# Kernel tuning notes

Measured on AMD Instinct MI355X. Metric: run time of the kernel, lower is better.

The kernel has to match this reference:

```python
import jax, jax.numpy as jnp
import numpy as np

B, D, K, UD, E, H = 2048, 256, 20, 512, 64, 256
HID = max(UD, 2 * E)  # FiLM hidden dim = 512
LN_EPS = 1e-5


def setup_inputs() -> dict:
    key = jax.random.key(0)
    ks = jax.random.split(key, 32)
    r = lambda i, shape, s=0.05: jax.random.normal(ks[i], shape, dtype=jnp.float32) * s
    inp = {
        'U': jax.random.normal(ks[0], (B, UD), dtype=jnp.float32),
        'X': jax.random.randint(ks[1], (B, D), 0, K, dtype=jnp.int32),
        # embedding table [K, E]
        'emb': r(2, (K, E), 1.0),
        # u0 linear: e0 = U @ u0_w.T + u0_b
        'u0_w': r(3, (E, UD)), 'u0_b': r(4, (E,)),
        # FiLM gamma branch: Linear(UD->HID), LayerNorm(HID), SiLU, Linear(HID->E)
        'gw1': r(5, (HID, UD)), 'gb1': r(6, (HID,)),
        'gln_w': jnp.ones((HID,), jnp.float32), 'gln_b': jnp.zeros((HID,), jnp.float32),
        'gw2': r(7, (E, HID)), 'gb2': r(8, (E,)),
        # FiLM beta branch
        'bw1': r(9, (HID, UD)), 'bb1': r(10, (HID,)),
        'bln_w': jnp.ones((HID,), jnp.float32), 'bln_b': jnp.zeros((HID,), jnp.float32),
        'bw2': r(11, (E, HID)), 'bb2': r(12, (E,)),
        # 2-layer LSTM (PyTorch gate order i,f,g,o)
        'wih0': r(13, (4 * H, E)), 'whh0': r(14, (4 * H, H)),
        'bih0': r(15, (4 * H,)), 'bhh0': r(16, (4 * H,)),
        'wih1': r(17, (4 * H, H)), 'whh1': r(18, (4 * H, H)),
        'bih1': r(19, (4 * H,)), 'bhh1': r(20, (4 * H,)),
        # output head: logits = h @ head_w.T + head_b
        'head_w': r(21, (K, H)), 'head_b': r(22, (K,)),
    }
    return inp


def _film_branch(u, w1, b1, lnw, lnb, w2, b2):
    h = u @ w1.T + b1
    mu = h.mean(-1, keepdims=True)
    var = ((h - mu) ** 2).mean(-1, keepdims=True)
    h = (h - mu) / jnp.sqrt(var + LN_EPS) * lnw + lnb
    return jax.nn.silu(h) @ w2.T + b2


def _lstm_cell(x, h, c, wih, whh, bih, bhh):
    g = x @ wih.T + bih + h @ whh.T + bhh
    i, f, gg, o = jnp.split(g, 4, axis=-1)
    c = jax.nn.sigmoid(f) * c + jax.nn.sigmoid(i) * jnp.tanh(gg)
    h = jax.nn.sigmoid(o) * jnp.tanh(c)
    return h, c


def reference(U, X, emb, u0_w, u0_b, gw1, gb1, gln_w, gln_b, gw2, gb2,
              bw1, bb1, bln_w, bln_b, bw2, bb2,
              wih0, whh0, bih0, bhh0, wih1, whh1, bih1, bhh1, head_w, head_b):
    # FiLM conditioning from context U
    gam = _film_branch(U, gw1, gb1, gln_w, gln_b, gw2, gb2)  # [B,E]
    bet = _film_branch(U, bw1, bb1, bln_w, bln_b, bw2, bb2)  # [B,E]
    e0 = U @ u0_w.T + u0_b                                   # [B,E] prefix embedding

    # Teacher-forced FiLM-modulated embeddings: e' = e*(1+gamma)+beta
    ex = emb[X] * (1.0 + gam[:, None, :]) + bet[:, None, :]  # [B,D,E]
    xs = jnp.concatenate([e0[:, None, :], ex[:, :-1]], axis=1)  # [B,D,E]
    xs = xs.transpose(1, 0, 2)  # [D,B,E]

    h0 = jnp.zeros((U.shape[0], H), xs.dtype)
    carry0 = (h0, h0, h0, h0)  # (h_l0, c_l0, h_l1, c_l1)

    def step(carry, x_t):
        h_0, c_0, h_1, c_1 = carry
        h_0, c_0 = _lstm_cell(x_t, h_0, c_0, wih0, whh0, bih0, bhh0)
        h_1, c_1 = _lstm_cell(h_0, h_1, c_1, wih1, whh1, bih1, bhh1)
        return (h_1 := h_1, c_1, h_1, c_1) if False else ((h_0, c_0, h_1, c_1), h_1)

    _, hs = jax.lax.scan(step, carry0, xs)  # [D,B,H]

    logits = jnp.einsum('dbh,kh->dbk', hs, head_w) + head_b  # [D,B,K]
    logp = jax.nn.log_softmax(logits, axis=-1)
    tok = X.T[:, :, None]  # [D,B,1]
    logq = jnp.take_along_axis(logp, tok, axis=-1).squeeze(-1).sum(0)  # [B]
    return logq
```

## Files before the change

### kernel.cpp

```cpp
#include <hip/hip_runtime.h>

#define B_   2048
#define D_   256
#define K_   20
#define UD_  512
#define E_   64
#define H_   256
#define HID_ 512

typedef __attribute__((ext_vector_type(8))) short bf8;
typedef __attribute__((ext_vector_type(4))) short s4;
typedef __attribute__((ext_vector_type(4))) float f32x4;
typedef __attribute__((ext_vector_type(4))) float f4;

#define MFMA16(a,b,c) __builtin_amdgcn_mfma_f32_16x16x32_bf16(a, b, c, 0, 0, 0)

#define GLD(dst, p)  asm volatile("global_load_dwordx4 %0, %1, off sc1" : "=v"(dst) : "v"(p))
#define GST2(p, v)   asm volatile("global_store_dwordx2 %0, %1, off sc1" :: "v"(p), "v"(v) : "memory")
#define GSTD(p, v)   asm volatile("global_store_dword %0, %1, off sc1" :: "v"(p), "v"(v) : "memory")
#define GLDD(dst, p) asm volatile("global_load_dword %0, %1, off sc1\n\ts_waitcnt vmcnt(0)" : "=v"(dst) : "v"(p) : "memory")

__device__ __forceinline__ unsigned short f2bf(float x) {
  unsigned u = __float_as_uint(x);
  u += 0x7fffu + ((u >> 16) & 1u);
  return (unsigned short)(u >> 16);
}
__device__ __forceinline__ float bfu(unsigned short x) {
  return __uint_as_float(((unsigned)x) << 16);
}
__device__ __forceinline__ float sigf(float x) {
  return __builtin_amdgcn_rcpf(1.0f + __expf(-x));
}
__device__ __forceinline__ float tanhf_(float x) {
  return 1.0f - 2.0f * __builtin_amdgcn_rcpf(__expf(2.0f * x) + 1.0f);
}

__global__ __launch_bounds__(256) void pack_w(const float* __restrict__ W,
    unsigned short* __restrict__ dst, int NT, int KTsrc, int KTtot, int kt0,
    int ldw, int Nsrc)
{
  int idx = blockIdx.x * 256 + threadIdx.x;
  int total = NT * KTsrc * 64;
  if (idx >= total) return;
  int l  = idx & 63;
  int fk = idx >> 6;
  int kt = fk % KTsrc;
  int nt = fk / KTsrc;
  int n = nt * 16 + (l & 15);
  int k = kt * 32 + ((l >> 4) * 8);
  bf8 o;
#pragma unroll
  for (int j = 0; j < 8; ++j)
    o[j] = (n < Nsrc) ? (short)f2bf(W[(size_t)n * ldw + k + j]) : (short)0;
  *(bf8*)(dst + (((size_t)(nt * KTtot + kt0 + kt)) * 64 + l) * 8) = o;
}

__global__ __launch_bounds__(256) void cvt_bf(const float* __restrict__ src,
    unsigned short* __restrict__ dst, int n8)
{
  int i = blockIdx.x * 256 + threadIdx.x;
  if (i >= n8) return;
  const f4* s = (const f4*)(src + (size_t)i * 8);
  f4 v0 = s[0], v1 = s[1];
  bf8 o;
#pragma unroll
  for (int j = 0; j < 4; ++j) { o[j] = (short)f2bf(v0[j]); o[4 + j] = (short)f2bf(v1[j]); }
  *(bf8*)(dst + (size_t)i * 8) = o;
}

template<bool OUTBF>
__global__ __launch_bounds__(256) void gemm_bt(
    const unsigned short* __restrict__ A, int lda, int aoff,
    const unsigned short* __restrict__ Bp, int KT,
    void* __restrict__ Cptr, int ldc, int coff,
    const float* __restrict__ bias)
{
  int tid = threadIdx.x;
  int l = tid & 63, w = tid >> 6;
  int wr = w >> 1, wc = w & 1;
  int r0 = blockIdx.y * 64 + wr * 32;
  int n0 = blockIdx.x * 64 + wc * 32;
  int lr = l & 15, lk = (l >> 4) * 8;
  f32x4 acc[2][2] = {};
  const unsigned short* a0p = A + (size_t)(r0 + lr) * lda + aoff + lk;
  const unsigned short* a1p = A + (size_t)(r0 + 16 + lr) * lda + aoff + lk;
  int ntb = n0 >> 4;
  for (int kt = 0; kt < KT; ++kt) {
    bf8 a0 = *(const bf8*)(a0p + kt * 32);
    bf8 a1 = *(const bf8*)(a1p + kt * 32);
    bf8 b0 = *(const bf8*)(Bp + (((size_t)(ntb + 0) * KT + kt) * 64 + l) * 8);
    bf8 b1 = *(const bf8*)(Bp + (((size_t)(ntb + 1) * KT + kt) * 64 + l) * 8);
    acc[0][0] = MFMA16(a0, b0, acc[0][0]);
    acc[0][1] = MFMA16(a0, b1, acc[0][1]);
    acc[1][0] = MFMA16(a1, b0, acc[1][0]);
    acc[1][1] = MFMA16(a1, b1, acc[1][1]);
  }
#pragma unroll
  for (int mi = 0; mi < 2; ++mi)
#pragma unroll
  for (int nj = 0; nj < 2; ++nj)
#pragma unroll
  for (int r = 0; r < 4; ++r) {
    int row = r0 + mi * 16 + (l >> 4) * 4 + r;
    int n = n0 + nj * 16 + lr;
    float v = acc[mi][nj][r] + bias[n];
    if (OUTBF) ((unsigned short*)Cptr)[(size_t)row * ldc + coff + n] = f2bf(v);
    else       ((float*)Cptr)[(size_t)row * ldc + coff + n] = v;
  }
}

__global__ __launch_bounds__(256) void ln_silu(
    const float* __restrict__ Hgb, unsigned short* __restrict__ Hsi,
    const float* __restrict__ gw, const float* __restrict__ gb,
    const float* __restrict__ bw, const float* __restrict__ bb)
{
  int tid = threadIdx.x;
  int l = tid & 63, w = tid >> 6;
  int gwv = blockIdx.x * 4 + w;
  int row = gwv >> 1, br = gwv & 1;
  const float* base = Hgb + (size_t)row * 1024 + br * 512 + l * 8;
  f4 v0 = *(const f4*)base;
  f4 v1 = *(const f4*)(base + 4);
  float s1 = 0.f, s2 = 0.f;
#pragma unroll
  for (int j = 0; j < 4; ++j) { s1 += v0[j] + v1[j]; s2 += v0[j] * v0[j] + v1[j] * v1[j]; }
  for (int m = 1; m < 64; m <<= 1) { s1 += __shfl_xor(s1, m, 64); s2 += __shfl_xor(s2, m, 64); }
  float mean = s1 * (1.0f / 512.0f);
  float var  = s2 * (1.0f / 512.0f) - mean * mean;
  float rstd = rsqrtf(var + 1e-5f);
  const float* W  = br ? bw : gw;
  const float* Bb = br ? bb : gb;
  bf8 o;
#pragma unroll
  for (int j = 0; j < 8; ++j) {
    float x = (j < 4) ? v0[j] : v1[j - 4];
    float y = (x - mean) * rstd * W[l * 8 + j] + Bb[l * 8 + j];
    o[j] = (short)f2bf(y * sigf(y));
  }
  *(bf8*)(Hsi + (size_t)row * 1024 + br * 512 + l * 8) = o;
}

struct PParams {
  const unsigned short* embB;
  const unsigned short* gbB;
  const unsigned short* E0;
  const unsigned short* W0p;
  const unsigned short* W1p;
  const unsigned short* Whp;
  unsigned short* H0;
  unsigned short* H1;
  unsigned* flags;
  const float* bih0; const float* bhh0;
  const float* bih1; const float* bhh1;
  const float* headb;
  const int* X;
  float* out;
};

__device__ __forceinline__ bf8 mod_frag(const unsigned short* e,
                                        const unsigned short* gb)
{
  bf8 ev = *(const bf8*)e;
  bf8 gv = *(const bf8*)gb;
  bf8 bv = *(const bf8*)(gb + 64);
  bf8 o;
#pragma unroll
  for (int j = 0; j < 8; ++j) {
    float x = bfu((unsigned short)ev[j]) * (1.0f + bfu((unsigned short)gv[j]))
            + bfu((unsigned short)bv[j]);
    o[j] = (short)f2bf(x);
  }
  return o;
}

__device__ __forceinline__ void group_barrier(unsigned* flags, int gid,
                                              int mem, unsigned target)
{
  asm volatile("s_waitcnt vmcnt(0)" ::: "memory");
  __syncthreads();
  if (threadIdx.x == 0) {
    GSTD(&flags[gid * 16 + mem], target);
  }
  int lane = threadIdx.x & 63;
  if (lane < 16 && lane != mem) {
    const unsigned* fp = &flags[gid * 16 + lane];
    unsigned v;
    GLDD(v, fp);
    while (v < target) {
      __builtin_amdgcn_s_sleep(1);
      GLDD(v, fp);
    }
  }
}

__global__ __launch_bounds__(512, 2) void persistent(PParams P)
{
  __shared__ __align__(16) unsigned short ldsw[120 * 512];
  __shared__ __align__(16) unsigned short tps[8][256];
  const int tid = threadIdx.x;
  const int l = tid & 63, w = tid >> 6;
  const int lr = l & 15, lk = (l >> 4) * 8;
  const int bx = blockIdx.x;
  const int gid = bx & 15;
  const int mem = bx >> 4;

  for (int f = w; f < 104; f += 8) {
    const unsigned short* src;
    if (f < 40) {
      int g = f / 10, kt = f - g * 10;
      src = P.W0p + (((size_t)((g * 16 + mem) * 10 + kt)) * 64 + l) * 8;
    } else {
      int f1 = f - 40; int g = f1 >> 4, kt = f1 & 15;
      src = P.W1p + (((size_t)((g * 16 + mem) * 16 + kt)) * 64 + l) * 8;
    }
    *(bf8*)(ldsw + (size_t)f * 512 + l * 8) = *(const bf8*)src;
  }
  for (int f = w; f < 16; f += 8)
    *(bf8*)(ldsw + (size_t)(104 + f) * 512 + l * 8) =
        *(const bf8*)(P.Whp + ((size_t)f * 64 + l) * 8);
  __syncthreads();

  const int r0 = gid * 128 + w * 16;
  const int c  = mem * 16 + lr;
  const size_t HN = (size_t)B_ * H_;
  const int rowA = r0 + lr;
  const int row2 = l & 15, ch2 = (l >> 4) & 3;
  const size_t strow = (size_t)(r0 + row2) * H_ + mem * 16 + ch2 * 4;
  unsigned short* tb = &tps[w][0];

  const float bi0 = P.bih0[c]           + P.bhh0[c];
  const float bf0 = P.bih0[H_ + c]      + P.bhh0[H_ + c];
  const float bg0 = P.bih0[2 * H_ + c]  + P.bhh0[2 * H_ + c];
  const float bo0 = P.bih0[3 * H_ + c]  + P.bhh0[3 * H_ + c];
  const float bi1 = P.bih1[c]           + P.bhh1[c];
  const float bf1 = P.bih1[H_ + c]      + P.bhh1[H_ + c];
  const float bg1 = P.bih1[2 * H_ + c]  + P.bhh1[2 * H_ + c];
  const float bo1 = P.bih1[3 * H_ + c]  + P.bhh1[3 * H_ + c];
  const float hb0 = P.headb[lr];
  const float hb1 = (lr < 4) ? P.headb[16 + lr] : 0.f;

  float c0r[4] = {};
  float c1r[4] = {};
  float lq[4]  = {};

  for (int ph = 0; ph <= 257; ++ph) {
    const unsigned short* h0r = P.H0 + ((size_t)((ph + 1) & 1)) * HN;
    unsigned short*       h0w = P.H0 + ((size_t)(ph & 1)) * HN;
    const unsigned short* h1r = P.H1 + ((size_t)(ph & 1)) * HN;
    unsigned short*       h1w = P.H1 + ((size_t)((ph + 1) & 1)) * HN;

    bf8 xa[2];
    if (ph < D_) {
      if (ph == 0) {
#pragma unroll
        for (int kt = 0; kt < 2; ++kt)
          xa[kt] = *(const bf8*)(P.E0 + (size_t)rowA * E_ + kt * 32 + lk);
      } else {
        int tok = P.X[rowA * D_ + ph - 1];
#pragma unroll
        for (int kt = 0; kt < 2; ++kt) {
          int k0 = kt * 32 + lk;
          xa[kt] = mod_frag(P.embB + tok * E_ + k0, P.gbB + (size_t)rowA * 128 + k0);
        }
      }
    }
    __builtin_amdgcn_sched_barrier(0);

    bf8 ha[8], h1a[8];
    {
      const unsigned short* pa = h0r + (size_t)rowA * H_ + lk;
#pragma unroll
      for (int kt = 0; kt < 8; ++kt) GLD(ha[kt], pa + kt * 32);
      const unsigned short* pb = h1r + (size_t)rowA * H_ + lk;
#pragma unroll
      for (int kt = 0; kt < 8; ++kt) GLD(h1a[kt], pb + kt * 32);
    }

    f32x4 acc0[4] = {};
    if (ph < D_) {
#pragma unroll
      for (int kt = 0; kt < 2; ++kt)
#pragma unroll
      for (int g = 0; g < 4; ++g) {
        bf8 b = *(const bf8*)(ldsw + (size_t)(g * 10 + kt) * 512 + l * 8);
        acc0[g] = MFMA16(xa[kt], b, acc0[g]);
      }
    }
    asm volatile("s_waitcnt vmcnt(8)" ::: "memory");
    __builtin_amdgcn_sched_barrier(0x100);

    bf8 hv0;
    if (ph < D_) {
#pragma unroll
      for (int kt = 2; kt < 10; ++kt)
#pragma unroll
      for (int g = 0; g < 4; ++g) {
        bf8 b = *(const bf8*)(ldsw + (size_t)(g * 10 + kt) * 512 + l * 8);
        acc0[g] = MFMA16(ha[kt - 2], b, acc0[g]);
      }
#pragma unroll
      for (int r = 0; r < 4; ++r) {
        float iv = sigf(acc0[0][r] + bi0);
        float fv = sigf(acc0[1][r] + bf0);
        float gv = tanhf_(acc0[2][r] + bg0);
        float ov = sigf(acc0[3][r] + bo0);
        float cn = fv * c0r[r] + iv * gv;
        c0r[r] = cn;
        tb[((l >> 4) * 4 + r) * 16 + lr] = f2bf(ov * tanhf_(cn));
      }
      asm volatile("s_waitcnt lgkmcnt(0)" ::: "memory");
      __builtin_amdgcn_sched_barrier(0);
      hv0 = *(const bf8*)(tb + row2 * 16 + ch2 * 4);
    }

    asm volatile("s_waitcnt vmcnt(0)" ::: "memory");
    __builtin_amdgcn_sched_barrier(0x100);
    if (ph < D_) {
      s4 sv = { hv0[0], hv0[1], hv0[2], hv0[3] };
      GST2(h0w + strow, sv);
    }

    if (ph >= 1 && ph <= 256) {
      f32x4 acc[4] = {};
#pragma unroll
      for (int kt = 0; kt < 16; ++kt) {
        bf8 a = (kt < 8) ? ha[kt] : h1a[kt - 8];
#pragma unroll
        for (int g = 0; g < 4; ++g) {
          bf8 b = *(const bf8*)(ldsw + (size_t)(40 + g * 16 + kt) * 512 + l * 8);
          acc[g] = MFMA16(a, b, acc[g]);
        }
      }
#pragma unroll
      for (int r = 0; r < 4; ++r) {
        float iv = sigf(acc[0][r] + bi1);
        float fv = sigf(acc[1][r] + bf1);
        float gv = tanhf_(acc[2][r] + bg1);
        float ov = sigf(acc[3][r] + bo1);
        float cn = fv * c1r[r] + iv * gv;
        c1r[r] = cn;
        tb[((l >> 4) * 4 + r) * 16 + lr] = f2bf(ov * tanhf_(cn));
      }
      asm volatile("s_waitcnt lgkmcnt(0)" ::: "memory");
      __builtin_amdgcn_sched_barrier(0);
      bf8 hv1 = *(const bf8*)(tb + row2 * 16 + ch2 * 4);
      s4 sv = { hv1[0], hv1[1], hv1[2], hv1[3] };
      GST2(h1w + strow, sv);
    }

    if (ph >= 2 && ((ph - 2) & 15) == mem) {
      const int th = ph - 2;
      f32x4 ac0 = {0,0,0,0}, ac1 = {0,0,0,0};
#pragma unroll
      for (int kt = 0; kt < 8; ++kt) {
        bf8 b0 = *(const bf8*)(ldsw + (size_t)(104 + kt) * 512 + l * 8);
        bf8 b1 = *(const bf8*)(ldsw + (size_t)(112 + kt) * 512 + l * 8);
        ac0 = MFMA16(h1a[kt], b0, ac0);
        ac1 = MFMA16(h1a[kt], b1, ac1);
      }
#pragma unroll
      for (int r = 0; r < 4; ++r) {
        int row = r0 + (l >> 4) * 4 + r;
        float v0 = ac0[r] + hb0;
        float v1 = (lr < 4) ? (ac1[r] + hb1) : -1e30f;
        float m = fmaxf(v0, v1);
#pragma unroll
        for (int msk = 1; msk < 16; msk <<= 1) m = fmaxf(m, __shfl_xor(m, msk, 64));
        float s = __expf(v0 - m) + ((lr < 4) ? __expf(v1 - m) : 0.f);
#pragma unroll
        for (int msk = 1; msk < 16; msk <<= 1) s += __shfl_xor(s, msk, 64);
        float lse = m + __logf(s);
        int tok = P.X[row * D_ + th];
        float lt = ((lr == tok) ? v0 : 0.f) + ((lr + 16 == tok) ? v1 : 0.f);
#pragma unroll
        for (int msk = 1; msk < 16; msk <<= 1) lt += __shfl_xor(lt, msk, 64);
        lq[r] += lt - lse;
      }
    }

    if (ph < 257) group_barrier(P.flags, gid, mem, (unsigned)(ph + 1));
  }

#pragma unroll
  for (int r = 0; r < 4; ++r) {
    int row = r0 + (l >> 4) * 4 + r;
    if (lr == 0) atomicAdd(&P.out[row], lq[r]);
  }
}

extern "C" void kernel_launch(void* const* d_in, const int* in_sizes, int n_in,
                              void* d_out, int out_size, void* d_ws, size_t ws_size,
                              hipStream_t stream)
{
  (void)in_sizes; (void)n_in; (void)ws_size;
  const float* U    = (const float*)d_in[0];
  const int*   X    = (const int*)  d_in[1];
  const float* emb  = (const float*)d_in[2];
  const float* u0w  = (const float*)d_in[3];
  const float* u0b  = (const float*)d_in[4];
  const float* gw1  = (const float*)d_in[5];
  const float* gb1  = (const float*)d_in[6];
  const float* glnw = (const float*)d_in[7];
  const float* glnb = (const float*)d_in[8];
  const float* gw2  = (const float*)d_in[9];
  const float* gb2  = (const float*)d_in[10];
  const float* bw1  = (const float*)d_in[11];
  const float* bb1  = (const float*)d_in[12];
  const float* blnw = (const float*)d_in[13];
  const float* blnb = (const float*)d_in[14];
  const float* bw2  = (const float*)d_in[15];
  const float* bb2  = (const float*)d_in[16];
  const float* wih0 = (const float*)d_in[17];
  const float* whh0 = (const float*)d_in[18];
  const float* bih0 = (const float*)d_in[19];
  const float* bhh0 = (const float*)d_in[20];
  const float* wih1 = (const float*)d_in[21];
  const float* whh1 = (const float*)d_in[22];
  const float* bih1 = (const float*)d_in[23];
  const float* bhh1 = (const float*)d_in[24];
  const float* headw = (const float*)d_in[25];
  const float* headb = (const float*)d_in[26];
  float* out = (float*)d_out;

  char* ws = (char*)d_ws;
  size_t off = 0;
  auto alloc = [&](size_t bytes) -> void* {
    void* p = ws + off; off += (bytes + 255) & ~(size_t)255; return p;
  };
  unsigned short* W0p  = (unsigned short*)alloc((size_t)1024 * 320 * 2);
  unsigned short* W1p  = (unsigned short*)alloc((size_t)1024 * 512 * 2);
  unsigned short* Wg1p = (unsigned short*)alloc((size_t)512 * 512 * 2);
  unsigned short* Wb1p = (unsigned short*)alloc((size_t)512 * 512 * 2);
  unsigned short* Wg2p = (unsigned short*)alloc((size_t)64 * 512 * 2);
  unsigned short* Wb2p = (unsigned short*)alloc((size_t)64 * 512 * 2);
  unsigned short* Wu0p = (unsigned short*)alloc((size_t)64 * 512 * 2);
  unsigned short* Whp  = (unsigned short*)alloc((size_t)32 * 256 * 2);
  unsigned short* Ubf  = (unsigned short*)alloc((size_t)B_ * UD_ * 2);
  float*          Hgb  = (float*)alloc((size_t)B_ * 1024 * 4);
  unsigned short* Hsi  = (unsigned short*)alloc((size_t)B_ * 1024 * 2);
  float*          GamBet = (float*)alloc((size_t)B_ * 128 * 4);
  unsigned short* GamBetB = (unsigned short*)alloc((size_t)B_ * 128 * 2);
  unsigned short* embB = (unsigned short*)alloc((size_t)K_ * E_ * 2);
  unsigned short* E0   = (unsigned short*)alloc((size_t)B_ * E_ * 2);
  size_t zoff = off;
  unsigned short* H0   = (unsigned short*)alloc((size_t)2 * B_ * H_ * 2);
  unsigned short* H1   = (unsigned short*)alloc((size_t)2 * B_ * H_ * 2);
  unsigned*       flags = (unsigned*)alloc((size_t)16 * 16 * sizeof(unsigned));
  size_t zbytes = off - zoff;

  hipMemsetAsync(ws + zoff, 0, zbytes, stream);
  hipMemsetAsync(out, 0, (size_t)out_size * sizeof(float), stream);

  auto pg = [](int tot) { return dim3((tot + 255) / 256); };
  pack_w<<<pg(64 * 2 * 64),  256, 0, stream>>>(wih0, W0p,  64,  2, 10, 0,  64, 1024);
  pack_w<<<pg(64 * 8 * 64),  256, 0, stream>>>(whh0, W0p,  64,  8, 10, 2, 256, 1024);
  pack_w<<<pg(64 * 8 * 64),  256, 0, stream>>>(wih1, W1p,  64,  8, 16, 0, 256, 1024);
  pack_w<<<pg(64 * 8 * 64),  256, 0, stream>>>(whh1, W1p,  64,  8, 16, 8, 256, 1024);
  pack_w<<<pg(32 * 16 * 64), 256, 0, stream>>>(gw1,  Wg1p, 32, 16, 16, 0, 512, 512);
  pack_w<<<pg(32 * 16 * 64), 256, 0, stream>>>(bw1,  Wb1p, 32, 16, 16, 0, 512, 512);
  pack_w<<<pg(4 * 16 * 64),  256, 0, stream>>>(gw2,  Wg2p,  4, 16, 16, 0, 512, 64);
  pack_w<<<pg(4 * 16 * 64),  256, 0, stream>>>(bw2,  Wb2p,  4, 16, 16, 0, 512, 64);
  pack_w<<<pg(4 * 16 * 64),  256, 0, stream>>>(u0w,  Wu0p,  4, 16, 16, 0, 512, 64);
  pack_w<<<pg(2 * 8 * 64),   256, 0, stream>>>(headw, Whp,  2,  8,  8, 0, 256, 20);
  cvt_bf<<<pg(B_ * UD_ / 8), 256, 0, stream>>>(U, Ubf, B_ * UD_ / 8);
  cvt_bf<<<pg(K_ * E_ / 8),  256, 0, stream>>>(emb, embB, K_ * E_ / 8);

  gemm_bt<false><<<dim3(8, 32), 256, 0, stream>>>(Ubf, UD_, 0, Wg1p, 16, Hgb, 1024, 0,   gb1);
  gemm_bt<false><<<dim3(8, 32), 256, 0, stream>>>(Ubf, UD_, 0, Wb1p, 16, Hgb, 1024, 512, bb1);
  ln_silu<<<1024, 256, 0, stream>>>(Hgb, Hsi, glnw, glnb, blnw, blnb);
  gemm_bt<false><<<dim3(1, 32), 256, 0, stream>>>(Hsi, 1024, 0,   Wg2p, 16, GamBet, 128, 0,  gb2);
  gemm_bt<false><<<dim3(1, 32), 256, 0, stream>>>(Hsi, 1024, 512, Wb2p, 16, GamBet, 128, 64, bb2);
  cvt_bf<<<pg(B_ * 128 / 8), 256, 0, stream>>>(GamBet, GamBetB, B_ * 128 / 8);
  gemm_bt<true><<<dim3(1, 32), 256, 0, stream>>>(Ubf, UD_, 0, Wu0p, 16, E0, E_, 0, u0b);

  PParams P;
  P.embB = embB; P.gbB = GamBetB; P.E0 = E0;
  P.W0p = W0p; P.W1p = W1p; P.Whp = Whp;
  P.H0 = H0; P.H1 = H1; P.flags = flags;
  P.bih0 = bih0; P.bhh0 = bhh0; P.bih1 = bih1; P.bhh1 = bhh1;
  P.headb = headb; P.X = X; P.out = out;
  persistent<<<dim3(256), dim3(512), 0, stream>>>(P);
}
```

Measured before the change: 2.722 ms.

## Split group barrier into per-layer flags and prefetch next-step hidden states

Replaces the single per-step group barrier with separate publish/wait flag sets for layer-0 and layer-1 hidden states, so each layer waits only on the data it needs. Next-step h0/h1 fragments and the modulated input embedding are loaded at the end of each step into double-buffered registers, with the loop unrolled by two to swap buffers. The aim is to shorten the serial critical path of the recurrent pipeline by overlapping global loads and finer-grained synchronisation with compute. In exchange it raises register pressure and makes the cross-block ordering more delicate to get right.

```diff
diff --git a/kernel.cpp b/kernel.cpp
--- a/kernel.cpp
+++ b/kernel.cpp
@@ -173,17 +173,17 @@
   return o;
 }
 
-__device__ __forceinline__ void group_barrier(unsigned* flags, int gid,
-                                              int mem, unsigned target)
+__device__ __forceinline__ void publish(unsigned* gf, int mem, unsigned target)
 {
   asm volatile("s_waitcnt vmcnt(0)" ::: "memory");
   __syncthreads();
-  if (threadIdx.x == 0) {
-    GSTD(&flags[gid * 16 + mem], target);
-  }
+  if (threadIdx.x == 0) GSTD(&gf[mem], target);
+}
+__device__ __forceinline__ void waitflags(unsigned* gf, int mem, unsigned target)
+{
   int lane = threadIdx.x & 63;
   if (lane < 16 && lane != mem) {
-    const unsigned* fp = &flags[gid * 16 + lane];
+    const unsigned* fp = &gf[lane];
     unsigned v;
     GLDD(v, fp);
     while (v < target) {
@@ -203,6 +203,8 @@
   const int bx = blockIdx.x;
   const int gid = bx & 15;
   const int mem = bx >> 4;
+  unsigned* h0f = P.flags + gid * 16;
+  unsigned* h1f = P.flags + 256 + gid * 16;
 
   for (int f = w; f < 104; f += 8) {
     const unsigned short* src;
@@ -243,88 +245,67 @@
   float c1r[4] = {};
   float lq[4]  = {};
 
-  for (int ph = 0; ph <= 257; ++ph) {
-    const unsigned short* h0r = P.H0 + ((size_t)((ph + 1) & 1)) * HN;
-    unsigned short*       h0w = P.H0 + ((size_t)(ph & 1)) * HN;
-    const unsigned short* h1r = P.H1 + ((size_t)(ph & 1)) * HN;
-    unsigned short*       h1w = P.H1 + ((size_t)((ph + 1) & 1)) * HN;
-
-    bf8 xa[2];
+  bf8 z8 = {};
+  bf8 haA[8], haB[8], h1A[8], h1B[8], xaA[2], xaB[2];
+#pragma unroll
+  for (int i = 0; i < 8; ++i) { haA[i] = z8; haB[i] = z8; h1A[i] = z8; h1B[i] = z8; }
+#pragma unroll
+  for (int kt = 0; kt < 2; ++kt)
+    xaA[kt] = *(const bf8*)(P.E0 + (size_t)rowA * E_ + kt * 32 + lk);
+  xaB[0] = z8; xaB[1] = z8;
+
+  auto body = [&](int ph, bf8 (&haC)[8], bf8 (&haN)[8],
+                          bf8 (&h1C)[8], bf8 (&h1N)[8],
+                          bf8 (&xaC)[2], bf8 (&xaN)[2]) {
+    unsigned short* h0wp = P.H0 + (size_t)(ph & 1) * HN;
+    unsigned short* h1wp = P.H1 + (size_t)((ph + 1) & 1) * HN;
+
     if (ph < D_) {
-      if (ph == 0) {
-#pragma unroll
-        for (int kt = 0; kt < 2; ++kt)
-          xa[kt] = *(const bf8*)(P.E0 + (size_t)rowA * E_ + kt * 32 + lk);
-      } else {
-        int tok = P.X[rowA * D_ + ph - 1];
-#pragma unroll
-        for (int kt = 0; kt < 2; ++kt) {
-          int k0 = kt * 32 + lk;
-          xa[kt] = mod_frag(P.embB + tok * E_ + k0, P.gbB + (size_t)rowA * 128 + k0);
-        }
-      }
-    }
-    __builtin_amdgcn_sched_barrier(0);
-
-    bf8 ha[8], h1a[8];
-    {
-      const unsigned short* pa = h0r + (size_t)rowA * H_ + lk;
-#pragma unroll
-      for (int kt = 0; kt < 8; ++kt) GLD(ha[kt], pa + kt * 32);
-      const unsigned short* pb = h1r + (size_t)rowA * H_ + lk;
-#pragma unroll
-      for (int kt = 0; kt < 8; ++kt) GLD(h1a[kt], pb + kt * 32);
-    }
-
-    f32x4 acc0[4] = {};
-    if (ph < D_) {
+      f32x4 acc[4] = {};
 #pragma unroll
       for (int kt = 0; kt < 2; ++kt)
 #pragma unroll
       for (int g = 0; g < 4; ++g) {
         bf8 b = *(const bf8*)(ldsw + (size_t)(g * 10 + kt) * 512 + l * 8);
-        acc0[g] = MFMA16(xa[kt], b, acc0[g]);
-      }
-    }
-    asm volatile("s_waitcnt vmcnt(8)" ::: "memory");
-    __builtin_amdgcn_sched_barrier(0x100);
-
-    bf8 hv0;
-    if (ph < D_) {
+        acc[g] = MFMA16(xaC[kt], b, acc[g]);
+      }
+      asm volatile("s_waitcnt vmcnt(8)" ::: "memory");
+      __builtin_amdgcn_sched_barrier(0x100);
 #pragma unroll
       for (int kt = 2; kt < 10; ++kt)
 #pragma unroll
       for (int g = 0; g < 4; ++g) {
         bf8 b = *(const bf8*)(ldsw + (size_t)(g * 10 + kt) * 512 + l * 8);
-        acc0[g] = MFMA16(ha[kt - 2], b, acc0[g]);
+        acc[g] = MFMA16(haC[kt - 2], b, acc[g]);
       }
 #pragma unroll
       for (int r = 0; r < 4; ++r) {
-        float iv = sigf(acc0[0][r] + bi0);
-        float fv = sigf(acc0[1][r] + bf0);
-        float gv = tanhf_(acc0[2][r] + bg0);
-        float ov = sigf(acc0[3][r] + bo0);
+        float iv = sigf(acc[0][r] + bi0);
+        float fv = sigf(acc[1][r] + bf0);
+        float gv = tanhf_(acc[2][r] + bg0);
+        float ov = sigf(acc[3][r] + bo0);
         float cn = fv * c0r[r] + iv * gv;
         c0r[r] = cn;
         tb[((l >> 4) * 4 + r) * 16 + lr] = f2bf(ov * tanhf_(cn));
       }
       asm volatile("s_waitcnt lgkmcnt(0)" ::: "memory");
       __builtin_amdgcn_sched_barrier(0);
-      hv0 = *(const bf8*)(tb + row2 * 16 + ch2 * 4);
-    }
-
-    asm volatile("s_waitcnt vmcnt(0)" ::: "memory");
-    __builtin_amdgcn_sched_barrier(0x100);
-    if (ph < D_) {
+      bf8 hv0 = *(const bf8*)(tb + row2 * 16 + ch2 * 4);
       s4 sv = { hv0[0], hv0[1], hv0[2], hv0[3] };
-      GST2(h0w + strow, sv);
-    }
-
-    if (ph >= 1 && ph <= 256) {
+      GST2(h0wp + strow, sv);
+      publish(h0f, mem, (unsigned)(ph + 1));
+      waitflags(h0f, mem, (unsigned)(ph + 1));
+      const unsigned short* pa = h0wp + (size_t)rowA * H_ + lk;
+#pragma unroll
+      for (int kt = 0; kt < 8; ++kt) GLD(haN[kt], pa + kt * 32);
+    }
+    if (ph >= D_) { asm volatile("s_waitcnt vmcnt(0)" ::: "memory"); }
+
+    if (ph >= 1 && ph <= D_) {
       f32x4 acc[4] = {};
 #pragma unroll
       for (int kt = 0; kt < 16; ++kt) {
-        bf8 a = (kt < 8) ? ha[kt] : h1a[kt - 8];
+        bf8 a = (kt < 8) ? haC[kt] : h1C[kt - 8];
 #pragma unroll
         for (int g = 0; g < 4; ++g) {
           bf8 b = *(const bf8*)(ldsw + (size_t)(40 + g * 16 + kt) * 512 + l * 8);
@@ -345,7 +326,8 @@
       __builtin_amdgcn_sched_barrier(0);
       bf8 hv1 = *(const bf8*)(tb + row2 * 16 + ch2 * 4);
       s4 sv = { hv1[0], hv1[1], hv1[2], hv1[3] };
-      GST2(h1w + strow, sv);
+      GST2(h1wp + strow, sv);
+      publish(h1f, mem, (unsigned)(ph + 1));
     }
 
     if (ph >= 2 && ((ph - 2) & 15) == mem) {
@@ -355,8 +337,8 @@
       for (int kt = 0; kt < 8; ++kt) {
         bf8 b0 = *(const bf8*)(ldsw + (size_t)(104 + kt) * 512 + l * 8);
         bf8 b1 = *(const bf8*)(ldsw + (size_t)(112 + kt) * 512 + l * 8);
-        ac0 = MFMA16(h1a[kt], b0, ac0);
-        ac1 = MFMA16(h1a[kt], b1, ac1);
+        ac0 = MFMA16(h1C[kt], b0, ac0);
+        ac1 = MFMA16(h1C[kt], b1, ac1);
       }
 #pragma unroll
       for (int r = 0; r < 4; ++r) {
@@ -378,7 +360,26 @@
       }
     }
 
-    if (ph < 257) group_barrier(P.flags, gid, mem, (unsigned)(ph + 1));
+    if (ph + 1 < D_) {
+      int tok = P.X[rowA * D_ + ph];
+#pragma unroll
+      for (int kt = 0; kt < 2; ++kt) {
+        int k0 = kt * 32 + lk;
+        xaN[kt] = mod_frag(P.embB + tok * E_ + k0, P.gbB + (size_t)rowA * 128 + k0);
+      }
+    }
+
+    if (ph >= 1 && ph <= D_) waitflags(h1f, mem, (unsigned)(ph + 1));
+    if (ph <= D_) {
+      const unsigned short* pb = h1wp + (size_t)rowA * H_ + lk;
+#pragma unroll
+      for (int kt = 0; kt < 8; ++kt) GLD(h1N[kt], pb + kt * 32);
+    }
+  };
+
+  for (int base = 0; base < 258; base += 2) {
+    body(base,     haA, haB, h1A, h1B, xaA, xaB);
+    body(base + 1, haB, haA, h1B, h1A, xaB, xaA);
   }
 
 #pragma unroll
@@ -445,7 +446,7 @@
   size_t zoff = off;
   unsigned short* H0   = (unsigned short*)alloc((size_t)2 * B_ * H_ * 2);
   unsigned short* H1   = (unsigned short*)alloc((size_t)2 * B_ * H_ * 2);
-  unsigned*       flags = (unsigned*)alloc((size_t)16 * 16 * sizeof(unsigned));
+  unsigned*       flags = (unsigned*)alloc((size_t)2 * 16 * 16 * sizeof(unsigned));
   size_t zbytes = off - zoff;
 
   hipMemsetAsync(ws + zoff, 0, zbytes, stream);
```

New measurement: 3.556 ms. 30.6% more time.

## Replace block-wide group barrier with per-wave split publish/wait flags

Applied to the files above, without the earlier changes.

Replaces the per-block __syncthreads plus single flag with per-wave flags: each wave publishes its step counter right after storing its h rows, then waits on the matching wave in the other 15 blocks of its group. The head/logprob work and the next step's FiLM-modulated input fetch now sit between publish and wait, so they overlap with peers' progress instead of running on the critical path. This trades a coarse block barrier for finer point-to-point sync, at the cost of 8x more flags and more polling traffic. Correctness relies on each wave only reading the rows its peer waves wrote.

```diff
diff --git a/kernel.cpp b/kernel.cpp
--- a/kernel.cpp
+++ b/kernel.cpp
@@ -173,17 +173,18 @@
   return o;
 }
 
-__device__ __forceinline__ void group_barrier(unsigned* flags, int gid,
-                                              int mem, unsigned target)
+__device__ __forceinline__ void publish_wave(unsigned* wf, int mem, int lane,
+                                             unsigned target)
 {
   asm volatile("s_waitcnt vmcnt(0)" ::: "memory");
-  __syncthreads();
-  if (threadIdx.x == 0) {
-    GSTD(&flags[gid * 16 + mem], target);
-  }
-  int lane = threadIdx.x & 63;
+  __builtin_amdgcn_sched_barrier(0);
+  if (lane == 0) GSTD(&wf[mem], target);
+}
+__device__ __forceinline__ void wait_wave(unsigned* wf, int mem, int lane,
+                                          unsigned target)
+{
   if (lane < 16 && lane != mem) {
-    const unsigned* fp = &flags[gid * 16 + lane];
+    const unsigned* fp = &wf[lane];
     unsigned v;
     GLDD(v, fp);
     while (v < target) {
@@ -203,6 +204,7 @@
   const int bx = blockIdx.x;
   const int gid = bx & 15;
   const int mem = bx >> 4;
+  unsigned* wf = P.flags + ((size_t)(gid * 8 + w)) * 16;
 
   for (int f = w; f < 104; f += 8) {
     const unsigned short* src;
@@ -243,28 +245,16 @@
   float c1r[4] = {};
   float lq[4]  = {};
 
+  bf8 xa[2];
+#pragma unroll
+  for (int kt = 0; kt < 2; ++kt)
+    xa[kt] = *(const bf8*)(P.E0 + (size_t)rowA * E_ + kt * 32 + lk);
+
   for (int ph = 0; ph <= 257; ++ph) {
     const unsigned short* h0r = P.H0 + ((size_t)((ph + 1) & 1)) * HN;
-    unsigned short*       h0w = P.H0 + ((size_t)(ph & 1)) * HN;
+    unsigned short*       h0wp = P.H0 + ((size_t)(ph & 1)) * HN;
     const unsigned short* h1r = P.H1 + ((size_t)(ph & 1)) * HN;
-    unsigned short*       h1w = P.H1 + ((size_t)((ph + 1) & 1)) * HN;
-
-    bf8 xa[2];
-    if (ph < D_) {
-      if (ph == 0) {
-#pragma unroll
-        for (int kt = 0; kt < 2; ++kt)
-          xa[kt] = *(const bf8*)(P.E0 + (size_t)rowA * E_ + kt * 32 + lk);
-      } else {
-        int tok = P.X[rowA * D_ + ph - 1];
-#pragma unroll
-        for (int kt = 0; kt < 2; ++kt) {
-          int k0 = kt * 32 + lk;
-          xa[kt] = mod_frag(P.embB + tok * E_ + k0, P.gbB + (size_t)rowA * 128 + k0);
-        }
-      }
-    }
-    __builtin_amdgcn_sched_barrier(0);
+    unsigned short*       h1wp = P.H1 + ((size_t)((ph + 1) & 1)) * HN;
 
     bf8 ha[8], h1a[8];
     {
@@ -289,7 +279,6 @@
     asm volatile("s_waitcnt vmcnt(8)" ::: "memory");
     __builtin_amdgcn_sched_barrier(0x100);
 
-    bf8 hv0;
     if (ph < D_) {
 #pragma unroll
       for (int kt = 2; kt < 10; ++kt)
@@ -308,16 +297,15 @@
         c0r[r] = cn;
         tb[((l >> 4) * 4 + r) * 16 + lr] = f2bf(ov * tanhf_(cn));
       }
-      asm volatile("s_waitcnt lgkmcnt(0)" ::: "memory");
-      __builtin_amdgcn_sched_barrier(0);
-      hv0 = *(const bf8*)(tb + row2 * 16 + ch2 * 4);
-    }
-
+    }
     asm volatile("s_waitcnt vmcnt(0)" ::: "memory");
     __builtin_amdgcn_sched_barrier(0x100);
     if (ph < D_) {
+      asm volatile("s_waitcnt lgkmcnt(0)" ::: "memory");
+      __builtin_amdgcn_sched_barrier(0);
+      bf8 hv0 = *(const bf8*)(tb + row2 * 16 + ch2 * 4);
       s4 sv = { hv0[0], hv0[1], hv0[2], hv0[3] };
-      GST2(h0w + strow, sv);
+      GST2(h0wp + strow, sv);
     }
 
     if (ph >= 1 && ph <= 256) {
@@ -345,8 +333,10 @@
       __builtin_amdgcn_sched_barrier(0);
       bf8 hv1 = *(const bf8*)(tb + row2 * 16 + ch2 * 4);
       s4 sv = { hv1[0], hv1[1], hv1[2], hv1[3] };
-      GST2(h1w + strow, sv);
-    }
+      GST2(h1wp + strow, sv);
+    }
+
+    if (ph < 257) publish_wave(wf, mem, l, (unsigned)(ph + 1));
 
     if (ph >= 2 && ((ph - 2) & 15) == mem) {
       const int th = ph - 2;
@@ -378,7 +368,16 @@
       }
     }
 
-    if (ph < 257) group_barrier(P.flags, gid, mem, (unsigned)(ph + 1));
+    if (ph + 1 < D_) {
+      int tok = P.X[rowA * D_ + ph];
+#pragma unroll
+      for (int kt = 0; kt < 2; ++kt) {
+        int k0 = kt * 32 + lk;
+        xa[kt] = mod_frag(P.embB + tok * E_ + k0, P.gbB + (size_t)rowA * 128 + k0);
+      }
+    }
+
+    if (ph < 257) wait_wave(wf, mem, l, (unsigned)(ph + 1));
   }
 
 #pragma unroll
@@ -445,7 +444,7 @@
   size_t zoff = off;
   unsigned short* H0   = (unsigned short*)alloc((size_t)2 * B_ * H_ * 2);
   unsigned short* H1   = (unsigned short*)alloc((size_t)2 * B_ * H_ * 2);
-  unsigned*       flags = (unsigned*)alloc((size_t)16 * 16 * sizeof(unsigned));
+  unsigned*       flags = (unsigned*)alloc((size_t)16 * 8 * 16 * sizeof(unsigned));
   size_t zbytes = off - zoff;
 
   hipMemsetAsync(ws + zoff, 0, zbytes, stream);
```

After: 2.603 ms. 4.4% less time.
